# Kernel tuning notes

Hardware: AMD Instinct MI355X
Metric: run time of the kernel (lower is better)

The kernel has to match this reference:

```python
import jax, jax.numpy as jnp
import numpy as np

N_EMBED = 1024
N_HEAD = 16
HEAD_DIM = N_EMBED // N_HEAD


def setup_inputs() -> dict:
    key = jax.random.key(0)
    ks = jax.random.split(key, 6)
    B, T, C = 4, 2048, N_EMBED
    scale = 1.0 / np.sqrt(C)
    x = jax.random.normal(ks[0], (B, T, C), dtype=jnp.float32)
    # torch nn.Linear weights are [out, in]; y = x @ W.T
    Wk = jax.random.normal(ks[1], (C, C), dtype=jnp.float32) * scale
    Wq = jax.random.normal(ks[2], (C, C), dtype=jnp.float32) * scale
    Wv = jax.random.normal(ks[3], (C, C), dtype=jnp.float32) * scale
    Wp = jax.random.normal(ks[4], (C, C), dtype=jnp.float32) * scale
    bp = jax.random.normal(ks[5], (C,), dtype=jnp.float32) * 0.01
    return {"x": x, "Wk": Wk, "Wq": Wq, "Wv": Wv, "Wp": Wp, "bp": bp}


def reference(x, Wk, Wq, Wv, Wp, bp):
    B, T, C = x.shape
    H, D = N_HEAD, HEAD_DIM
    # QKV projections (torch Linear: x @ W.T), split heads -> [B, H, T, D]
    k = (x @ Wk.T).reshape(B, T, H, D).transpose(0, 2, 1, 3)
    q = (x @ Wq.T).reshape(B, T, H, D).transpose(0, 2, 1, 3)
    v = (x @ Wv.T).reshape(B, T, H, D).transpose(0, 2, 1, 3)
    # scaled scores [B, H, T, T]
    att = jnp.einsum('bhtd,bhsd->bhts', q, k) * (1.0 / np.sqrt(D))
    causal = jnp.tril(jnp.ones((T, T), dtype=bool))
    att = jnp.where(causal[None, None, :, :], att, -jnp.inf)
    att = jax.nn.softmax(att, axis=-1)
    out = jnp.einsum('bhts,bhsd->bhtd', att, v)  # [B, H, T, D]
    out = out.transpose(0, 2, 1, 3).reshape(B, T, C)
    out = out @ Wp.T + bp
    return out
```

## Files before the change

### kernel.cpp

```cpp
#include <hip/hip_runtime.h>

typedef __bf16 bf16_t;
typedef bf16_t bf16x4 __attribute__((ext_vector_type(4)));
typedef bf16_t bf16x8 __attribute__((ext_vector_type(8)));
typedef float f32x4 __attribute__((ext_vector_type(4)));

#define B_ 4
#define T_ 2048
#define C_ 1024
#define H_ 16
#define D_ 64

#define GLDS(g, l)                                                          \
  __builtin_amdgcn_global_load_lds(                                         \
      (const __attribute__((address_space(1))) void*)(g),                   \
      (__attribute__((address_space(3))) void*)(l), 16, 0, 0)

static __device__ __forceinline__ f32x4 mfma16(bf16x8 a, bf16x8 b, f32x4 c) {
  return __builtin_amdgcn_mfma_f32_16x16x32_bf16(a, b, c, 0, 0, 0);
}

__global__ void cvt_all(const float* __restrict__ x, const float* __restrict__ wq,
                        const float* __restrict__ wk, const float* __restrict__ wv,
                        const float* __restrict__ wp, bf16_t* __restrict__ xb,
                        bf16_t* __restrict__ wqb, bf16_t* __restrict__ wkb,
                        bf16_t* __restrict__ wvb, bf16_t* __restrict__ wpb) {
  int i = blockIdx.x * blockDim.x + threadIdx.x;
  const float* src;
  bf16_t* dst;
  int off;
  if (i < 2097152) {
    src = x; dst = xb; off = i;
  } else {
    int r = i - 2097152;
    int region = r >> 18;
    off = r & 262143;
    if (region == 0) { src = wq; dst = wqb; }
    else if (region == 1) { src = wk; dst = wkb; }
    else if (region == 2) { src = wv; dst = wvb; }
    else { src = wp; dst = wpb; }
  }
  float4 v = ((const float4*)src)[off];
  bf16x4 o = {(bf16_t)v.x, (bf16_t)v.y, (bf16_t)v.z, (bf16_t)v.w};
  ((bf16x4*)dst)[off] = o;
}

__device__ __forceinline__ void gemm_mainloop(const bf16_t* __restrict__ A,
                                              const bf16_t* __restrict__ W,
                                              bf16_t* lA, bf16_t* lB, int row0,
                                              int col0, f32x4 (&acc)[4][4]) {
  const int tid = threadIdx.x;
  const int wave = tid >> 6, lane = tid & 63;
  const int wr = wave >> 1, wc = wave & 1;
  for (int k0 = 0; k0 < C_; k0 += 64) {
#pragma unroll
    for (int it = 0; it < 4; ++it) {
      const int off = (it * 4 + wave) * 1024;
      const int lin = off + lane * 16;
      const int r = lin >> 7;
      const int c = ((lin >> 4) & 7) ^ (r & 7);
      GLDS(A + (size_t)(row0 + r) * C_ + k0 + c * 8, lA + (off >> 1));
      GLDS(W + (size_t)(col0 + r) * C_ + k0 + c * 8, lB + (off >> 1));
    }
    __syncthreads();
#pragma unroll
    for (int s = 0; s < 2; ++s) {
      bf16x8 af[4], bfr[4];
#pragma unroll
      for (int m = 0; m < 4; ++m) {
        const int r = wr * 64 + m * 16 + (lane & 15);
        const int c = s * 4 + (lane >> 4);
        af[m] = *(const bf16x8*)((const char*)lA + r * 128 +
                                 ((c ^ (r & 7)) << 4));
      }
#pragma unroll
      for (int n = 0; n < 4; ++n) {
        const int r = wc * 64 + n * 16 + (lane & 15);
        const int c = s * 4 + (lane >> 4);
        bfr[n] = *(const bf16x8*)((const char*)lB + r * 128 +
                                  ((c ^ (r & 7)) << 4));
      }
#pragma unroll
      for (int m = 0; m < 4; ++m)
#pragma unroll
        for (int n = 0; n < 4; ++n) acc[m][n] = mfma16(af[m], bfr[n], acc[m][n]);
    }
    __syncthreads();
  }
}

__global__ __launch_bounds__(256) void gemm_qkv(
    const bf16_t* __restrict__ xb, const bf16_t* __restrict__ wq,
    const bf16_t* __restrict__ wk, const bf16_t* __restrict__ wv,
    bf16_t* __restrict__ qo, bf16_t* __restrict__ ko, bf16_t* __restrict__ vt) {
  __shared__ bf16_t lA[128 * 64];
  __shared__ bf16_t lB[128 * 64];
  const int z = blockIdx.z;
  const bf16_t* W = (z == 0) ? wq : ((z == 1) ? wk : wv);
  bf16_t* outb = (z == 0) ? qo : ((z == 1) ? ko : vt);
  const int row0 = blockIdx.y * 128, col0 = blockIdx.x * 128;
  f32x4 acc[4][4] = {};
  gemm_mainloop(xb, W, lA, lB, row0, col0, acc);
  const int lane = threadIdx.x & 63, wave = threadIdx.x >> 6;
  const int wr = wave >> 1, wc = wave & 1;
  const float qs = (z == 0) ? 0.125f : 1.0f;
#pragma unroll
  for (int m = 0; m < 4; ++m) {
#pragma unroll
    for (int n = 0; n < 4; ++n) {
      const int gr = row0 + wr * 64 + m * 16 + ((lane >> 4) << 2);
      const int gc = col0 + wc * 64 + n * 16 + (lane & 15);
      const int b = gr >> 11, t = gr & (T_ - 1);
      const int h = gc >> 6, d = gc & 63;
      if (z < 2) {
#pragma unroll
        for (int j = 0; j < 4; ++j)
          outb[(((size_t)(b * H_ + h)) * T_ + (t + j)) * D_ + d] =
              (bf16_t)(acc[m][n][j] * qs);
      } else {
        bf16x4 pk = {(bf16_t)acc[m][n][0], (bf16_t)acc[m][n][1],
                     (bf16_t)acc[m][n][2], (bf16_t)acc[m][n][3]};
        *(bf16x4*)(outb + (((size_t)(b * H_ + h)) * D_ + d) * T_ + t) = pk;
      }
    }
  }
}

__global__ __launch_bounds__(256) void gemm_proj(const bf16_t* __restrict__ att,
                                                 const bf16_t* __restrict__ wp,
                                                 const float* __restrict__ bias,
                                                 float* __restrict__ out) {
  __shared__ bf16_t lA[128 * 64];
  __shared__ bf16_t lB[128 * 64];
  const int row0 = blockIdx.y * 128, col0 = blockIdx.x * 128;
  f32x4 acc[4][4] = {};
  gemm_mainloop(att, wp, lA, lB, row0, col0, acc);
  const int lane = threadIdx.x & 63, wave = threadIdx.x >> 6;
  const int wr = wave >> 1, wc = wave & 1;
#pragma unroll
  for (int m = 0; m < 4; ++m) {
#pragma unroll
    for (int n = 0; n < 4; ++n) {
      const int gr = row0 + wr * 64 + m * 16 + ((lane >> 4) << 2);
      const int gc = col0 + wc * 64 + n * 16 + (lane & 15);
      const float bv = bias[gc];
#pragma unroll
      for (int j = 0; j < 4; ++j)
        out[(size_t)(gr + j) * C_ + gc] = acc[m][n][j] + bv;
    }
  }
}

__global__ __launch_bounds__(512, 4) void attn_fwd(
    const bf16_t* __restrict__ Q, const bf16_t* __restrict__ K,
    const bf16_t* __restrict__ V, bf16_t* __restrict__ AO) {
  __shared__ bf16_t lK[2][64 * 64];
  __shared__ bf16_t lV[2][64 * 64];
  __shared__ bf16_t lP[8][16 * 64];
  const int tid = threadIdx.x, wave = tid >> 6, lane = tid & 63;
  const int g = lane >> 4;
  const int bh = blockIdx.y;
  const size_t baseK = (size_t)bh * T_ * D_;
  const size_t baseV = (size_t)bh * D_ * T_;
  const int bb = bh >> 4, hh = bh & 15;

  for (int half = 0; half < 2; ++half) {
    const int qt = half ? (15 - blockIdx.x) : blockIdx.x;
    const int twv = qt * 128 + wave * 16;
    const int ntiles = 2 * qt + 2;
    __syncthreads();
    {
      const int off = wave * 1024;
      const int lin = off + lane * 16;
      const int r = lin >> 7;
      const int c = ((lin >> 4) & 7) ^ (r & 7);
      GLDS(K + baseK + (size_t)r * D_ + c * 8, &lK[0][off >> 1]);
      GLDS(V + baseV + (size_t)r * T_ + c * 8, &lV[0][off >> 1]);
    }
    bf16x8 qf[2];
#pragma unroll
    for (int s = 0; s < 2; ++s)
      qf[s] = *(const bf16x8*)(Q + baseK +
                               (size_t)(twv + (lane & 15)) * D_ + s * 32 +
                               (g << 3));
    float mrun = -1e30f, lrun = 0.f;
    f32x4 o[4] = {};
    int cur = 0;
    for (int it = 0; it < ntiles; ++it) {
      __syncthreads();
      if (it + 1 < ntiles) {
        const int s0n = (it + 1) * 64;
        const int nb = cur ^ 1;
        const int off = wave * 1024;
        const int lin = off + lane * 16;
        const int r = lin >> 7;
        const int c = ((lin >> 4) & 7) ^ (r & 7);
        GLDS(K + baseK + (size_t)(s0n + r) * D_ + c * 8, &lK[nb][off >> 1]);
        GLDS(V + baseV + (size_t)r * T_ + s0n + c * 8, &lV[nb][off >> 1]);
      }
      const int s0 = it * 64;
      f32x4 sc[4];
#pragma unroll
      for (int nf = 0; nf < 4; ++nf) sc[nf] = (f32x4){};
      __builtin_amdgcn_s_setprio(1);
#pragma unroll
      for (int s = 0; s < 2; ++s) {
#pragma unroll
        for (int nf = 0; nf < 4; ++nf) {
          const int r = nf * 16 + (lane & 15);
          const int c = s * 4 + g;
          bf16x8 kf = *(const bf16x8*)((const char*)lK[cur] + r * 128 +
                                       ((c ^ (r & 7)) << 4));
          sc[nf] = mfma16(kf, qf[s], sc[nf]);
        }
      }
      __builtin_amdgcn_s_setprio(0);
      if (it >= 2 * qt) {
        const int t = twv + (lane & 15);
#pragma unroll
        for (int nf = 0; nf < 4; ++nf)
#pragma unroll
          for (int j = 0; j < 4; ++j) {
            const int s = s0 + nf * 16 + g * 4 + j;
            if (s > t) sc[nf][j] = -1e30f;
          }
      }
      float pmax = sc[0][0];
#pragma unroll
      for (int nf = 0; nf < 4; ++nf)
#pragma unroll
        for (int j = 0; j < 4; ++j) pmax = fmaxf(pmax, sc[nf][j]);
      pmax = fmaxf(pmax, __shfl_xor(pmax, 16));
      pmax = fmaxf(pmax, __shfl_xor(pmax, 32));
      const float mn = fmaxf(mrun, pmax);
      const float scl = __expf(mrun - mn);
      mrun = mn;
      float ps = 0.f;
      bf16x4 pk[4];
#pragma unroll
      for (int nf = 0; nf < 4; ++nf)
#pragma unroll
        for (int j = 0; j < 4; ++j) {
          const float p = __expf(sc[nf][j] - mn);
          ps += p;
          pk[nf][j] = (bf16_t)p;
        }
      ps += __shfl_xor(ps, 16);
      ps += __shfl_xor(ps, 32);
      lrun = lrun * scl + ps;
      float sb[4];
#pragma unroll
      for (int j = 0; j < 4; ++j)
        sb[j] = __shfl(scl, (lane & 48) | ((g << 2) + j));
#pragma unroll
      for (int df = 0; df < 4; ++df)
#pragma unroll
        for (int j = 0; j < 4; ++j) o[df][j] *= sb[j];
      {
        const int r = lane & 15;
#pragma unroll
        for (int nf = 0; nf < 4; ++nf)
          *(bf16x4*)((char*)lP[wave] + r * 128 +
                     ((((2 * nf + (g >> 1)) ^ (r & 7)) << 4) |
                      ((g & 1) << 3))) = pk[nf];
      }
      __builtin_amdgcn_s_setprio(1);
#pragma unroll
      for (int s2 = 0; s2 < 2; ++s2) {
        const int cp = s2 * 4 + g;
        const int rp = lane & 15;
        bf16x8 pf = *(const bf16x8*)((const char*)lP[wave] + rp * 128 +
                                     ((cp ^ (rp & 7)) << 4));
#pragma unroll
        for (int df = 0; df < 4; ++df) {
          const int rv = df * 16 + (lane & 15);
          bf16x8 vf = *(const bf16x8*)((const char*)lV[cur] + rv * 128 +
                                       ((cp ^ (rv & 7)) << 4));
          o[df] = mfma16(pf, vf, o[df]);
        }
      }
      __builtin_amdgcn_s_setprio(0);
      cur ^= 1;
    }
    {
      const float inv = 1.0f / lrun;
      float ib[4];
#pragma unroll
      for (int j = 0; j < 4; ++j)
        ib[j] = __shfl(inv, (lane & 48) | ((g << 2) + j));
#pragma unroll
      for (int j = 0; j < 4; ++j) {
        const int t = twv + (g << 2) + j;
#pragma unroll
        for (int df = 0; df < 4; ++df) {
          const int cc = hh * 64 + df * 16 + (lane & 15);
          AO[((size_t)(bb * T_ + t)) * C_ + cc] = (bf16_t)(o[df][j] * ib[j]);
        }
      }
    }
  }
}

extern "C" void kernel_launch(void* const* d_in, const int* in_sizes, int n_in,
                              void* d_out, int out_size, void* d_ws,
                              size_t ws_size, hipStream_t stream) {
  const float* x = (const float*)d_in[0];
  const float* Wk = (const float*)d_in[1];
  const float* Wq = (const float*)d_in[2];
  const float* Wv = (const float*)d_in[3];
  const float* Wp = (const float*)d_in[4];
  const float* bp = (const float*)d_in[5];
  char* ws = (char*)d_ws;
  bf16_t* xb = (bf16_t*)ws;
  bf16_t* wqb = (bf16_t*)(ws + (16u << 20));
  bf16_t* wkb = (bf16_t*)(ws + (18u << 20));
  bf16_t* wvb = (bf16_t*)(ws + (20u << 20));
  bf16_t* wpb = (bf16_t*)(ws + (22u << 20));
  bf16_t* q = (bf16_t*)(ws + (24u << 20));
  bf16_t* k = (bf16_t*)(ws + (40u << 20));
  bf16_t* vt = (bf16_t*)(ws + (56u << 20));
  bf16_t* att = xb;

  cvt_all<<<12288, 256, 0, stream>>>(x, Wq, Wk, Wv, Wp, xb, wqb, wkb, wvb, wpb);
  gemm_qkv<<<dim3(8, 64, 3), 256, 0, stream>>>(xb, wqb, wkb, wvb, q, k, vt);
  attn_fwd<<<dim3(8, 64), 512, 0, stream>>>(q, k, vt, att);
  gemm_proj<<<dim3(8, 64), 256, 0, stream>>>(att, wpb, bp, (float*)d_out);
}
```

Before: 191.1 us.

## Fuse Q/K/V projections into one block sharing the loaded X tile

The QKV GEMM now computes all three projections in one 512-thread block that loads the X tile into LDS once and reuses it against three weight tiles, instead of launching a separate block per projection. Each wave computes a 64x32 sub-tile for each of Q, K and V. A swizzled 1D block index groups neighbouring column tiles. This cuts redundant global and LDS traffic for X, at the cost of more LDS (four 16KB tiles), 96 accumulators per thread, and fewer blocks (512 instead of 1536).

```diff
diff --git a/kernel.cpp b/kernel.cpp
--- a/kernel.cpp
+++ b/kernel.cpp
@@ -45,6 +45,87 @@
   ((bf16x4*)dst)[off] = o;
 }
 
+__global__ __launch_bounds__(512) void gemm_qkv(
+    const bf16_t* __restrict__ xb, const bf16_t* __restrict__ wq,
+    const bf16_t* __restrict__ wk, const bf16_t* __restrict__ wv,
+    bf16_t* __restrict__ qo, bf16_t* __restrict__ ko, bf16_t* __restrict__ vt) {
+  __shared__ bf16_t lA[128 * 64];
+  __shared__ bf16_t lB[3][128 * 64];
+  const int tid = threadIdx.x, wave = tid >> 6, lane = tid & 63;
+  const int g = lane >> 4;
+  const int bid = blockIdx.x;
+  const int swz = ((bid & 7) << 6) | (bid >> 3);
+  const int col0 = (swz & 7) * 128, row0 = (swz >> 3) * 128;
+  const int wr = wave >> 2, wc = wave & 3;
+  f32x4 acc[3][4][2] = {};
+  for (int k0 = 0; k0 < C_; k0 += 64) {
+#pragma unroll
+    for (int i = 0; i < 2; ++i) {
+      const int off = (i * 8 + wave) * 1024;
+      const int lin = off + lane * 16;
+      const int r = lin >> 7;
+      const int c = ((lin >> 4) & 7) ^ (r & 7);
+      GLDS(xb + (size_t)(row0 + r) * C_ + k0 + c * 8, lA + (off >> 1));
+      GLDS(wq + (size_t)(col0 + r) * C_ + k0 + c * 8, &lB[0][off >> 1]);
+      GLDS(wk + (size_t)(col0 + r) * C_ + k0 + c * 8, &lB[1][off >> 1]);
+      GLDS(wv + (size_t)(col0 + r) * C_ + k0 + c * 8, &lB[2][off >> 1]);
+    }
+    __syncthreads();
+#pragma unroll
+    for (int s = 0; s < 2; ++s) {
+      const int c = s * 4 + g;
+      bf16x8 af[4];
+#pragma unroll
+      for (int m = 0; m < 4; ++m) {
+        const int r = wr * 64 + m * 16 + (lane & 15);
+        af[m] = *(const bf16x8*)((const char*)lA + r * 128 +
+                                 ((c ^ (r & 7)) << 4));
+      }
+#pragma unroll
+      for (int z = 0; z < 3; ++z) {
+        bf16x8 bfr[2];
+#pragma unroll
+        for (int n = 0; n < 2; ++n) {
+          const int r = wc * 32 + n * 16 + (lane & 15);
+          bfr[n] = *(const bf16x8*)((const char*)lB[z] + r * 128 +
+                                    ((c ^ (r & 7)) << 4));
+        }
+#pragma unroll
+        for (int m = 0; m < 4; ++m)
+#pragma unroll
+          for (int n = 0; n < 2; ++n)
+            acc[z][m][n] = mfma16(af[m], bfr[n], acc[z][m][n]);
+      }
+    }
+    __syncthreads();
+  }
+#pragma unroll
+  for (int z = 0; z < 3; ++z) {
+    bf16_t* outb = (z == 0) ? qo : ((z == 1) ? ko : vt);
+    const float qs = (z == 0) ? 0.125f : 1.0f;
+#pragma unroll
+    for (int m = 0; m < 4; ++m) {
+#pragma unroll
+      for (int n = 0; n < 2; ++n) {
+        const int gr = row0 + wr * 64 + m * 16 + ((lane >> 4) << 2);
+        const int gc = col0 + wc * 32 + n * 16 + (lane & 15);
+        const int b = gr >> 11, t = gr & (T_ - 1);
+        const int h = gc >> 6, d = gc & 63;
+        if (z < 2) {
+#pragma unroll
+          for (int j = 0; j < 4; ++j)
+            outb[(((size_t)(b * H_ + h)) * T_ + (t + j)) * D_ + d] =
+                (bf16_t)(acc[z][m][n][j] * qs);
+        } else {
+          bf16x4 pk = {(bf16_t)acc[z][m][n][0], (bf16_t)acc[z][m][n][1],
+                       (bf16_t)acc[z][m][n][2], (bf16_t)acc[z][m][n][3]};
+          *(bf16x4*)(outb + (((size_t)(b * H_ + h)) * D_ + d) * T_ + t) = pk;
+        }
+      }
+    }
+  }
+}
+
 __device__ __forceinline__ void gemm_mainloop(const bf16_t* __restrict__ A,
                                               const bf16_t* __restrict__ W,
                                               bf16_t* lA, bf16_t* lB, int row0,
@@ -86,43 +167,6 @@
         for (int n = 0; n < 4; ++n) acc[m][n] = mfma16(af[m], bfr[n], acc[m][n]);
     }
     __syncthreads();
-  }
-}
-
-__global__ __launch_bounds__(256) void gemm_qkv(
-    const bf16_t* __restrict__ xb, const bf16_t* __restrict__ wq,
-    const bf16_t* __restrict__ wk, const bf16_t* __restrict__ wv,
-    bf16_t* __restrict__ qo, bf16_t* __restrict__ ko, bf16_t* __restrict__ vt) {
-  __shared__ bf16_t lA[128 * 64];
-  __shared__ bf16_t lB[128 * 64];
-  const int z = blockIdx.z;
-  const bf16_t* W = (z == 0) ? wq : ((z == 1) ? wk : wv);
-  bf16_t* outb = (z == 0) ? qo : ((z == 1) ? ko : vt);
-  const int row0 = blockIdx.y * 128, col0 = blockIdx.x * 128;
-  f32x4 acc[4][4] = {};
-  gemm_mainloop(xb, W, lA, lB, row0, col0, acc);
-  const int lane = threadIdx.x & 63, wave = threadIdx.x >> 6;
-  const int wr = wave >> 1, wc = wave & 1;
-  const float qs = (z == 0) ? 0.125f : 1.0f;
-#pragma unroll
-  for (int m = 0; m < 4; ++m) {
-#pragma unroll
-    for (int n = 0; n < 4; ++n) {
-      const int gr = row0 + wr * 64 + m * 16 + ((lane >> 4) << 2);
-      const int gc = col0 + wc * 64 + n * 16 + (lane & 15);
-      const int b = gr >> 11, t = gr & (T_ - 1);
-      const int h = gc >> 6, d = gc & 63;
-      if (z < 2) {
-#pragma unroll
-        for (int j = 0; j < 4; ++j)
-          outb[(((size_t)(b * H_ + h)) * T_ + (t + j)) * D_ + d] =
-              (bf16_t)(acc[m][n][j] * qs);
-      } else {
-        bf16x4 pk = {(bf16_t)acc[m][n][0], (bf16_t)acc[m][n][1],
-                     (bf16_t)acc[m][n][2], (bf16_t)acc[m][n][3]};
-        *(bf16x4*)(outb + (((size_t)(b * H_ + h)) * D_ + d) * T_ + t) = pk;
-      }
-    }
   }
 }
 
@@ -322,7 +366,7 @@
   bf16_t* att = xb;
 
   cvt_all<<<12288, 256, 0, stream>>>(x, Wq, Wk, Wv, Wp, xb, wqb, wkb, wvb, wpb);
-  gemm_qkv<<<dim3(8, 64, 3), 256, 0, stream>>>(xb, wqb, wkb, wvb, q, k, vt);
+  gemm_qkv<<<512, 512, 0, stream>>>(xb, wqb, wkb, wvb, q, k, vt);
   attn_fwd<<<dim3(8, 64), 512, 0, stream>>>(q, k, vt, att);
   gemm_proj<<<dim3(8, 64), 256, 0, stream>>>(att, wpb, bp, (float*)d_out);
 }
```

Result: faster. 179.8 us (-5.9%).
